# Performance work log

Hardware: AMD Instinct MI355X
Metric: run time of the kernel (lower is better)

Reference implementation:

```python
import jax, jax.numpy as jnp
import numpy as np

B = 131072
D_IN = 128
D_H = 128


def _linear_params(key, fan_in, fan_out):
    # mimic nn.Linear init: U(-1/sqrt(fan_in), 1/sqrt(fan_in))
    kw, kb = jax.random.split(key)
    bound = 1.0 / np.sqrt(fan_in)
    W = jax.random.uniform(kw, (fan_in, fan_out), minval=-bound, maxval=bound, dtype=jnp.float32)
    b = jax.random.uniform(kb, (fan_out,), minval=-bound, maxval=bound, dtype=jnp.float32)
    return W, b


def setup_inputs() -> dict:
    key = jax.random.key(0)
    ks = jax.random.split(key, 12)
    inp = {
        'input': jax.random.normal(ks[0], (B, D_IN), dtype=jnp.float32),
        'seq_input': jax.random.normal(ks[1], (B, D_IN), dtype=jnp.float32),
        'hidden': jax.random.normal(ks[2], (B, D_H), dtype=jnp.float32),
    }
    names = ['ir', 'iz', 'in_', 'sr', 'sz', 'sn', 'hr', 'hz', 'hn']
    for i, nm in enumerate(names):
        fan_in = D_H if nm.startswith('h') else D_IN
        W, b = _linear_params(ks[3 + i], fan_in, D_H)
        inp['W_' + nm] = W
        inp['b_' + nm] = b
    return inp


def reference(input, seq_input, hidden,
              W_ir, b_ir, W_iz, b_iz, W_in_, b_in_,
              W_sr, b_sr, W_sz, b_sz, W_sn, b_sn,
              W_hr, b_hr, W_hz, b_hz, W_hn, b_hn):
    def lin(x, W, b):
        return x @ W + b

    hr = lin(hidden, W_hr, b_hr)  # shared between r_input and r_seq
    r_input = jax.nn.sigmoid(lin(input, W_ir, b_ir) + hr)
    r_seq = jax.nn.sigmoid(lin(seq_input, W_sr, b_sr) + hr)
    r = (r_input + r_seq) * 0.5

    hz = lin(hidden, W_hz, b_hz)
    z_input = jax.nn.sigmoid(lin(input, W_iz, b_iz) + hz)
    z_seq = jax.nn.sigmoid(lin(seq_input, W_sz, b_sz) + hz)
    z = (z_input + z_seq) * 0.5

    n = jnp.tanh(lin(input, W_in_, b_in_) + lin(seq_input, W_sn, b_sn)
                 + lin(r * hidden, W_hn, b_hn))
    new_hidden = (1.0 - z) * n + z * hidden
    return new_hidden
```

## Files before the change

### kernel.cpp

```cpp
#include <hip/hip_runtime.h>

#define BDIM 512
#define PACK_BDIM 256

typedef __attribute__((ext_vector_type(8))) short bf16x8;
typedef __attribute__((ext_vector_type(4))) float f32x4;
typedef __attribute__((ext_vector_type(4))) unsigned int u32x4;

__device__ __forceinline__ unsigned short f2b(float x) {
    unsigned u = __float_as_uint(x);
    return (unsigned short)((u + 0x7fffu + ((u >> 16) & 1u)) >> 16);
}

typedef __attribute__((address_space(1))) const unsigned int ga_u32;
typedef __attribute__((address_space(3))) unsigned int la_u32;
__device__ __forceinline__ void gload_lds16(const void* g, void* l) {
    __builtin_amdgcn_global_load_lds((ga_u32*)g, (la_u32*)l, 16, 0, 0);
}

__global__ __launch_bounds__(PACK_BDIM) void pack_weights(
    const float* __restrict__ w0, const float* __restrict__ w1,
    const float* __restrict__ w2, const float* __restrict__ w3,
    const float* __restrict__ w4, const float* __restrict__ w5,
    const float* __restrict__ w6, const float* __restrict__ w7,
    const float* __restrict__ w8,
    const float* __restrict__ b0, const float* __restrict__ b1,
    const float* __restrict__ b2, const float* __restrict__ b3,
    const float* __restrict__ b4, const float* __restrict__ b5,
    const float* __restrict__ b6, const float* __restrict__ b7,
    const float* __restrict__ b8, unsigned short* __restrict__ wp)
{
    __shared__ float wsm[16384];
    const float* W; const float* Bp;
    switch (blockIdx.x) {
        case 0: W = w0; Bp = b0; break; case 1: W = w1; Bp = b1; break;
        case 2: W = w2; Bp = b2; break; case 3: W = w3; Bp = b3; break;
        case 4: W = w4; Bp = b4; break; case 5: W = w5; Bp = b5; break;
        case 6: W = w6; Bp = b6; break; case 7: W = w7; Bp = b7; break;
        default: W = w8; Bp = b8; break;
    }
    const int tid = threadIdx.x;
    for (int i = tid; i < 16384; i += PACK_BDIM) wsm[i] = W[i];
    float* biasf = (float*)(wp + 147456);
    if (tid < 128) biasf[blockIdx.x * 128 + tid] = Bp[tid];
    __syncthreads();
    unsigned short* dst = wp + (size_t)blockIdx.x * 16384;
    for (int item = tid; item < 2048; item += PACK_BDIM) {
        const int lane = item & 63, cf = item >> 6;
        const int c = cf >> 3, f = cf & 7;
        const int k0 = c * 32 + (lane >> 4) * 8;
        const int n  = f * 16 + (lane & 15);
        u32x4 vv;
        for (int i2 = 0; i2 < 4; i2++) {
            unsigned short lo = f2b(wsm[(k0 + 2 * i2)     * 128 + n]);
            unsigned short hi = f2b(wsm[(k0 + 2 * i2 + 1) * 128 + n]);
            vv[i2] = (unsigned)lo | ((unsigned)hi << 16);
        }
        *(u32x4*)(dst + (size_t)cf * 512 + lane * 8) = vv;
    }
}

__global__ __launch_bounds__(BDIM) __attribute__((amdgpu_waves_per_eu(4)))
void gru_fused(
    const float* __restrict__ inp, const float* __restrict__ seqp,
    const float* __restrict__ hid, const unsigned short* __restrict__ wp,
    float* __restrict__ outp)
{
    __shared__ __align__(16) unsigned short wbuf[2][16384];
    float* tbR = (float*)wbuf[1];
    float* tbO = (float*)wbuf[0];

    const int tid    = threadIdx.x;
    const int lane   = tid & 63;
    const int wid    = tid >> 6;
    const int rowgrp = wid >> 1;
    const int colgrp = wid & 1;
    const int agrp   = lane >> 4;
    const int a16    = lane & 15;
    const int ncol0  = colgrp * 64;
    const size_t row0 = (size_t)blockIdx.x * 64;
    const int locrow_a = rowgrp * 16 + a16;
    const int rswA = (locrow_a & 7) << 3;

    const float* pAin  = inp  + (row0 + locrow_a) * 128;
    const float* pAseq = seqp + (row0 + locrow_a) * 128;
    const float* pAhid = hid  + (row0 + locrow_a) * 128;
    const float* biasf = (const float*)(wp + 147456);

    f32x4 hx[4], s1[4], nacc[4], G[4];
    const f32x4 zv = {0.f, 0.f, 0.f, 0.f};

    auto stageu = [&](int g, int b) {
        const char* src = (const char*)wp + (size_t)g * 32768;
        char* dstb = (char*)wbuf[b];
        #pragma unroll
        for (int j = 0; j < 4; j++) {
            const int off = (j * 8 + wid) * 1024;
            gload_lds16(src + off + lane * 16, dstb + off);
        }
    };

    auto splitc2 = [&](f32x4 x0, f32x4 x1, bf16x8& ah, bf16x8& al) {
        u32x4 a, l;
        #pragma unroll
        for (int p = 0; p < 2; p++) {
            unsigned e0 = __float_as_uint(x0[2 * p]);
            unsigned e1 = __float_as_uint(x0[2 * p + 1]);
            a[p] = __builtin_amdgcn_perm(e1, e0, 0x07060302u);
            float d0 = x0[2 * p]     - __uint_as_float(e0 & 0xffff0000u);
            float d1 = x0[2 * p + 1] - __uint_as_float(e1 & 0xffff0000u);
            l[p] = __builtin_amdgcn_perm(__float_as_uint(d1), __float_as_uint(d0), 0x07060302u);
            unsigned f0 = __float_as_uint(x1[2 * p]);
            unsigned f1 = __float_as_uint(x1[2 * p + 1]);
            a[2 + p] = __builtin_amdgcn_perm(f1, f0, 0x07060302u);
            float g0 = x1[2 * p]     - __uint_as_float(f0 & 0xffff0000u);
            float g1 = x1[2 * p + 1] - __uint_as_float(f1 & 0xffff0000u);
            l[2 + p] = __builtin_amdgcn_perm(__float_as_uint(g1), __float_as_uint(g0), 0x07060302u);
        }
        ah = *(const bf16x8*)&a;
        al = *(const bf16x8*)&l;
    };

    auto gemmG = [&](int b, const float* pA, int g) {
        #pragma unroll
        for (int f = 0; f < 4; f++) G[f] = zv;
        const unsigned short* wb = wbuf[b];
        #pragma unroll
        for (int c = 0; c < 4; c++) {
            const float* p = pA + c * 32 + agrp * 8;
            bf16x8 ah, al;
            splitc2(*(const f32x4*)(p), *(const f32x4*)(p + 4), ah, al);
            __builtin_amdgcn_s_setprio(1);
            #pragma unroll
            for (int f = 0; f < 4; f++) {
                const int fglob = colgrp * 4 + f;
                const bf16x8 w = *(const bf16x8*)(&wb[(size_t)(c * 8 + fglob) * 512 + lane * 8]);
                G[f] = __builtin_amdgcn_mfma_f32_16x16x32_bf16(ah, w, G[f], 0, 0, 0);
                G[f] = __builtin_amdgcn_mfma_f32_16x16x32_bf16(al, w, G[f], 0, 0, 0);
            }
            __builtin_amdgcn_s_setprio(0);
        }
        #pragma unroll
        for (int f = 0; f < 4; f++) {
            float bv = biasf[g * 128 + ncol0 + f * 16 + a16];
            #pragma unroll
            for (int j = 0; j < 4; j++) G[f][j] += bv;
        }
    };

    auto gemmL = [&](int g) {
        #pragma unroll
        for (int f = 0; f < 4; f++) G[f] = zv;
        const unsigned short* wb = wbuf[0];
        #pragma unroll
        for (int c = 0; c < 4; c++) {
            const int rk = (c * 32 + agrp * 8) ^ rswA;
            f32x4 x0 = *(const f32x4*)(&tbR[locrow_a * 128 + rk]);
            f32x4 x1 = *(const f32x4*)(&tbR[locrow_a * 128 + rk + 4]);
            bf16x8 ah, al;
            splitc2(x0, x1, ah, al);
            __builtin_amdgcn_s_setprio(1);
            #pragma unroll
            for (int f = 0; f < 4; f++) {
                const int fglob = colgrp * 4 + f;
                const bf16x8 w = *(const bf16x8*)(&wb[(size_t)(c * 8 + fglob) * 512 + lane * 8]);
                G[f] = __builtin_amdgcn_mfma_f32_16x16x32_bf16(ah, w, G[f], 0, 0, 0);
                G[f] = __builtin_amdgcn_mfma_f32_16x16x32_bf16(al, w, G[f], 0, 0, 0);
            }
            __builtin_amdgcn_s_setprio(0);
        }
        #pragma unroll
        for (int f = 0; f < 4; f++) {
            float bv = biasf[g * 128 + ncol0 + f * 16 + a16];
            #pragma unroll
            for (int j = 0; j < 4; j++) G[f][j] += bv;
        }
    };

    auto sigm = [](float x) { return 1.f / (1.f + __expf(-x)); };
    auto tanh_ = [](float x) {
        x = fminf(18.f, fmaxf(-18.f, x));
        float e = __expf(2.f * x);
        return (e - 1.f) / (e + 1.f);
    };

    const unsigned long long GT = 0x417528306ULL;
    const unsigned CBT = 0x152u;
    stageu(6, 0);

    #pragma clang loop unroll(disable)
    for (int u = 0; u < 9; ++u) {
        const int g = (int)((GT >> (4 * u)) & 15);
        __syncthreads();
        if (u == 3) {
            gemmL(g);
        } else {
            if (u != 2 && u != 8)
                stageu((int)((GT >> (4 * (u + 1))) & 15), (CBT >> (u + 1)) & 1);
            const float* pA = (u == 0 || u == 6) ? pAhid
                            : (u == 1 || u == 4 || u == 7) ? pAin : pAseq;
            gemmG((CBT >> u) & 1, pA, g);
        }
        switch (u) {
            case 0: case 6:
                #pragma unroll
                for (int f = 0; f < 4; f++) hx[f] = G[f];
                break;
            case 1: case 7:
                #pragma unroll
                for (int f = 0; f < 4; f++)
                    #pragma unroll
                    for (int j = 0; j < 4; j++)
                        s1[f][j] = sigm(G[f][j] + hx[f][j]);
                break;
            case 2: {
                #pragma unroll
                for (int f = 0; f < 4; f++)
                    #pragma unroll
                    for (int j = 0; j < 4; j++) {
                        int row = rowgrp * 16 + agrp * 4 + j;
                        int col = ncol0 + f * 16 + a16;
                        float r = 0.5f * (s1[f][j] + sigm(G[f][j] + hx[f][j]));
                        float h = hid[(row0 + row) * 128 + col];
                        tbR[row * 128 + (col ^ ((row & 7) << 3))] = r * h;
                    }
                break;
            }
            case 3:
                #pragma unroll
                for (int f = 0; f < 4; f++) nacc[f] = G[f];
                break;
            case 4: case 5:
                #pragma unroll
                for (int f = 0; f < 4; f++) nacc[f] += G[f];
                break;
            default:
                break;
        }
        if (u == 2) { __syncthreads(); stageu(8, 0); }
        if (u == 3) { __syncthreads(); stageu(2, 1); }
    }

    #pragma unroll
    for (int f = 0; f < 4; f++)
        #pragma unroll
        for (int j = 0; j < 4; j++) {
            int row = rowgrp * 16 + agrp * 4 + j;
            int col = ncol0 + f * 16 + a16;
            float zz = 0.5f * (s1[f][j] + sigm(G[f][j] + hx[f][j]));
            float h  = hid[(row0 + row) * 128 + col];
            float nn = tanh_(nacc[f][j]);
            tbO[row * 128 + (col ^ ((row & 7) << 3))] = (1.f - zz) * nn + zz * h;
        }
    __syncthreads();
    #pragma unroll
    for (int p = 0; p < 4; p++) {
        int e = p * 2048 + tid * 4;
        int rrow = e >> 7, c0 = e & 127;
        f32x4 v = *(const f32x4*)(&tbO[rrow * 128 + (c0 ^ ((rrow & 7) << 3))]);
        *(f32x4*)(&outp[(row0 + rrow) * 128 + c0]) = v;
    }
}

extern "C" void kernel_launch(void* const* d_in, const int* in_sizes, int n_in,
                              void* d_out, int out_size, void* d_ws, size_t ws_size,
                              hipStream_t stream)
{
    (void)in_sizes; (void)n_in; (void)out_size; (void)ws_size;
    const float* inp  = (const float*)d_in[0];
    const float* seqp = (const float*)d_in[1];
    const float* hid  = (const float*)d_in[2];
    const float* W[9]; const float* Bv[9];
    for (int i = 0; i < 9; i++) {
        W[i]  = (const float*)d_in[3 + 2 * i];
        Bv[i] = (const float*)d_in[4 + 2 * i];
    }
    unsigned short* wp = (unsigned short*)d_ws;

    pack_weights<<<9, PACK_BDIM, 0, stream>>>(W[0], W[1], W[2], W[3], W[4],
                                              W[5], W[6], W[7], W[8],
                                              Bv[0], Bv[1], Bv[2], Bv[3], Bv[4],
                                              Bv[5], Bv[6], Bv[7], Bv[8], wp);
    gru_fused<<<2048, BDIM, 0, stream>>>(inp, seqp, hid, wp, (float*)d_out);
}
```

Before: 302.4 us.

## Switch GEMMs from 16x16x32 to 32x32x16 bf16 MFMA tiles

Rewrites the per-wave GEMM tiling to use 32x32x16 MFMA instructions. Each wave now owns a 32-row by 32-column tile instead of 16 rows by 64 columns. The weight pack layout and the epilogue row/column mapping change to match. The aim is fewer A-operand loads and bf16 hi/lo splits per MFMA, and fewer LDS weight reads per wave. In exchange each wave issues a serial chain of 16 dependent MFMAs on a single accumulator, and the s_setprio hints are removed.

```diff
diff --git a/kernel.cpp b/kernel.cpp
--- a/kernel.cpp
+++ b/kernel.cpp
@@ -5,6 +5,7 @@
 
 typedef __attribute__((ext_vector_type(8))) short bf16x8;
 typedef __attribute__((ext_vector_type(4))) float f32x4;
+typedef __attribute__((ext_vector_type(16))) float f32x16;
 typedef __attribute__((ext_vector_type(4))) unsigned int u32x4;
 
 __device__ __forceinline__ unsigned short f2b(float x) {
@@ -46,17 +47,17 @@
     __syncthreads();
     unsigned short* dst = wp + (size_t)blockIdx.x * 16384;
     for (int item = tid; item < 2048; item += PACK_BDIM) {
-        const int lane = item & 63, cf = item >> 6;
-        const int c = cf >> 3, f = cf & 7;
-        const int k0 = c * 32 + (lane >> 4) * 8;
-        const int n  = f * 16 + (lane & 15);
+        const int lane = item & 63, q = item >> 6;
+        const int s = q >> 2, F = q & 3;
+        const int k0 = s * 16 + (lane >> 5) * 8;
+        const int n  = F * 32 + (lane & 31);
         u32x4 vv;
         for (int i2 = 0; i2 < 4; i2++) {
             unsigned short lo = f2b(wsm[(k0 + 2 * i2)     * 128 + n]);
             unsigned short hi = f2b(wsm[(k0 + 2 * i2 + 1) * 128 + n]);
             vv[i2] = (unsigned)lo | ((unsigned)hi << 16);
         }
-        *(u32x4*)(dst + (size_t)cf * 512 + lane * 8) = vv;
+        *(u32x4*)(dst + (size_t)q * 512 + lane * 8) = vv;
     }
 }
 
@@ -73,22 +74,23 @@
     const int tid    = threadIdx.x;
     const int lane   = tid & 63;
     const int wid    = tid >> 6;
-    const int rowgrp = wid >> 1;
-    const int colgrp = wid & 1;
-    const int agrp   = lane >> 4;
-    const int a16    = lane & 15;
-    const int ncol0  = colgrp * 64;
+    const int rowgrp = wid >> 2;
+    const int colgrp = wid & 3;
+    const int l31    = lane & 31;
+    const int kgrp   = lane >> 5;
     const size_t row0 = (size_t)blockIdx.x * 64;
-    const int locrow_a = rowgrp * 16 + a16;
+    const int locrow_a = rowgrp * 32 + l31;
     const int rswA = (locrow_a & 7) << 3;
+    const int ocol = colgrp * 32 + l31;
 
     const float* pAin  = inp  + (row0 + locrow_a) * 128;
     const float* pAseq = seqp + (row0 + locrow_a) * 128;
     const float* pAhid = hid  + (row0 + locrow_a) * 128;
     const float* biasf = (const float*)(wp + 147456);
 
-    f32x4 hx[4], s1[4], nacc[4], G[4];
-    const f32x4 zv = {0.f, 0.f, 0.f, 0.f};
+    f32x16 hx, s1, nacc, G;
+    const f32x16 zv = {0.f,0.f,0.f,0.f,0.f,0.f,0.f,0.f,
+                       0.f,0.f,0.f,0.f,0.f,0.f,0.f,0.f};
 
     auto stageu = [&](int g, int b) {
         const char* src = (const char*)wp + (size_t)g * 32768;
@@ -122,59 +124,39 @@
     };
 
     auto gemmG = [&](int b, const float* pA, int g) {
-        #pragma unroll
-        for (int f = 0; f < 4; f++) G[f] = zv;
+        G = zv;
         const unsigned short* wb = wbuf[b];
         #pragma unroll
-        for (int c = 0; c < 4; c++) {
-            const float* p = pA + c * 32 + agrp * 8;
+        for (int s = 0; s < 8; s++) {
+            const float* p = pA + s * 16 + kgrp * 8;
             bf16x8 ah, al;
-            splitc2(*(const f32x4*)(p), *(const f32x4*)(p + 4), ah, al);
-            __builtin_amdgcn_s_setprio(1);
-            #pragma unroll
-            for (int f = 0; f < 4; f++) {
-                const int fglob = colgrp * 4 + f;
-                const bf16x8 w = *(const bf16x8*)(&wb[(size_t)(c * 8 + fglob) * 512 + lane * 8]);
-                G[f] = __builtin_amdgcn_mfma_f32_16x16x32_bf16(ah, w, G[f], 0, 0, 0);
-                G[f] = __builtin_amdgcn_mfma_f32_16x16x32_bf16(al, w, G[f], 0, 0, 0);
-            }
-            __builtin_amdgcn_s_setprio(0);
-        }
-        #pragma unroll
-        for (int f = 0; f < 4; f++) {
-            float bv = biasf[g * 128 + ncol0 + f * 16 + a16];
-            #pragma unroll
-            for (int j = 0; j < 4; j++) G[f][j] += bv;
-        }
+            splitc2(*(const f32x4*)p, *(const f32x4*)(p + 4), ah, al);
+            const bf16x8 w = *(const bf16x8*)(&wb[(size_t)(s * 4 + colgrp) * 512 + lane * 8]);
+            G = __builtin_amdgcn_mfma_f32_32x32x16_bf16(ah, w, G, 0, 0, 0);
+            G = __builtin_amdgcn_mfma_f32_32x32x16_bf16(al, w, G, 0, 0, 0);
+        }
+        const float bv = biasf[g * 128 + ocol];
+        #pragma unroll
+        for (int r = 0; r < 16; r++) G[r] += bv;
     };
 
     auto gemmL = [&](int g) {
-        #pragma unroll
-        for (int f = 0; f < 4; f++) G[f] = zv;
+        G = zv;
         const unsigned short* wb = wbuf[0];
         #pragma unroll
-        for (int c = 0; c < 4; c++) {
-            const int rk = (c * 32 + agrp * 8) ^ rswA;
+        for (int s = 0; s < 8; s++) {
+            const int rk = (s * 16 + kgrp * 8) ^ rswA;
             f32x4 x0 = *(const f32x4*)(&tbR[locrow_a * 128 + rk]);
             f32x4 x1 = *(const f32x4*)(&tbR[locrow_a * 128 + rk + 4]);
             bf16x8 ah, al;
             splitc2(x0, x1, ah, al);
-            __builtin_amdgcn_s_setprio(1);
-            #pragma unroll
-            for (int f = 0; f < 4; f++) {
-                const int fglob = colgrp * 4 + f;
-                const bf16x8 w = *(const bf16x8*)(&wb[(size_t)(c * 8 + fglob) * 512 + lane * 8]);
-                G[f] = __builtin_amdgcn_mfma_f32_16x16x32_bf16(ah, w, G[f], 0, 0, 0);
-                G[f] = __builtin_amdgcn_mfma_f32_16x16x32_bf16(al, w, G[f], 0, 0, 0);
-            }
-            __builtin_amdgcn_s_setprio(0);
-        }
-        #pragma unroll
-        for (int f = 0; f < 4; f++) {
-            float bv = biasf[g * 128 + ncol0 + f * 16 + a16];
-            #pragma unroll
-            for (int j = 0; j < 4; j++) G[f][j] += bv;
-        }
+            const bf16x8 w = *(const bf16x8*)(&wb[(size_t)(s * 4 + colgrp) * 512 + lane * 8]);
+            G = __builtin_amdgcn_mfma_f32_32x32x16_bf16(ah, w, G, 0, 0, 0);
+            G = __builtin_amdgcn_mfma_f32_32x32x16_bf16(al, w, G, 0, 0, 0);
+        }
+        const float bv = biasf[g * 128 + ocol];
+        #pragma unroll
+        for (int r = 0; r < 16; r++) G[r] += bv;
     };
 
     auto sigm = [](float x) { return 1.f / (1.f + __expf(-x)); };
@@ -203,36 +185,28 @@
         }
         switch (u) {
             case 0: case 6:
-                #pragma unroll
-                for (int f = 0; f < 4; f++) hx[f] = G[f];
+                hx = G;
                 break;
             case 1: case 7:
                 #pragma unroll
-                for (int f = 0; f < 4; f++)
-                    #pragma unroll
-                    for (int j = 0; j < 4; j++)
-                        s1[f][j] = sigm(G[f][j] + hx[f][j]);
+                for (int r = 0; r < 16; r++) s1[r] = sigm(G[r] + hx[r]);
                 break;
             case 2: {
                 #pragma unroll
-                for (int f = 0; f < 4; f++)
-                    #pragma unroll
-                    for (int j = 0; j < 4; j++) {
-                        int row = rowgrp * 16 + agrp * 4 + j;
-                        int col = ncol0 + f * 16 + a16;
-                        float r = 0.5f * (s1[f][j] + sigm(G[f][j] + hx[f][j]));
-                        float h = hid[(row0 + row) * 128 + col];
-                        tbR[row * 128 + (col ^ ((row & 7) << 3))] = r * h;
-                    }
+                for (int r = 0; r < 16; r++) {
+                    int row = rowgrp * 32 + (r & 3) + 8 * (r >> 2) + 4 * kgrp;
+                    float rr = 0.5f * (s1[r] + sigm(G[r] + hx[r]));
+                    float h = hid[(row0 + row) * 128 + ocol];
+                    tbR[row * 128 + (ocol ^ ((row & 7) << 3))] = rr * h;
+                }
                 break;
             }
             case 3:
-                #pragma unroll
-                for (int f = 0; f < 4; f++) nacc[f] = G[f];
+                nacc = G;
                 break;
             case 4: case 5:
                 #pragma unroll
-                for (int f = 0; f < 4; f++) nacc[f] += G[f];
+                for (int r = 0; r < 16; r++) nacc[r] += G[r];
                 break;
             default:
                 break;
@@ -242,16 +216,13 @@
     }
 
     #pragma unroll
-    for (int f = 0; f < 4; f++)
-        #pragma unroll
-        for (int j = 0; j < 4; j++) {
-            int row = rowgrp * 16 + agrp * 4 + j;
-            int col = ncol0 + f * 16 + a16;
-            float zz = 0.5f * (s1[f][j] + sigm(G[f][j] + hx[f][j]));
-            float h  = hid[(row0 + row) * 128 + col];
-            float nn = tanh_(nacc[f][j]);
-            tbO[row * 128 + (col ^ ((row & 7) << 3))] = (1.f - zz) * nn + zz * h;
-        }
+    for (int r = 0; r < 16; r++) {
+        int row = rowgrp * 32 + (r & 3) + 8 * (r >> 2) + 4 * kgrp;
+        float zz = 0.5f * (s1[r] + sigm(G[r] + hx[r]));
+        float h  = hid[(row0 + row) * 128 + ocol];
+        float nn = tanh_(nacc[r]);
+        tbO[row * 128 + (ocol ^ ((row & 7) << 3))] = (1.f - zz) * nn + zz * h;
+    }
     __syncthreads();
     #pragma unroll
     for (int p = 0; p < 4; p++) {
```

Measured after the change: 438.1 us. +44.9%, slower.

## Restructure GRU kernel into 1024-thread blocks with per-wave row tiles and three-slot weight staging

Applied to the files above, without the earlier changes.

Blocks grow to 1024 threads covering 256 rows, and each wave now owns 16 full rows across all 128 columns. Three gate weight matrices are staged into LDS at once, in three phases (r gates, n gates, z gates). The r*h product is kept in registers as a packed hi/lo bf16 pair and moved between lane layouts through per-wave LDS slices, so no block-wide tile exchange is needed. The n value is stored as fp16 until the final combine, and output is written through small per-wave LDS transposes. The aim is to amortise each weight load over more rows and cut block-wide syncs, at the cost of fewer resident blocks and higher register and LDS pressure. Storing n in fp16 also adds a small precision loss.

```diff
diff --git a/kernel.cpp b/kernel.cpp
--- a/kernel.cpp
+++ b/kernel.cpp
@@ -1,11 +1,12 @@
 #include <hip/hip_runtime.h>
 
-#define BDIM 512
+#define BDIM 1024
 #define PACK_BDIM 256
 
 typedef __attribute__((ext_vector_type(8))) short bf16x8;
 typedef __attribute__((ext_vector_type(4))) float f32x4;
 typedef __attribute__((ext_vector_type(4))) unsigned int u32x4;
+typedef __attribute__((ext_vector_type(2))) __fp16 f16x2;
 
 __device__ __forceinline__ unsigned short f2b(float x) {
     unsigned u = __float_as_uint(x);
@@ -66,37 +67,32 @@
     const float* __restrict__ hid, const unsigned short* __restrict__ wp,
     float* __restrict__ outp)
 {
-    __shared__ __align__(16) unsigned short wbuf[2][16384];
-    float* tbR = (float*)wbuf[1];
-    float* tbO = (float*)wbuf[0];
-
-    const int tid    = threadIdx.x;
-    const int lane   = tid & 63;
-    const int wid    = tid >> 6;
-    const int rowgrp = wid >> 1;
-    const int colgrp = wid & 1;
-    const int agrp   = lane >> 4;
-    const int a16    = lane & 15;
-    const int ncol0  = colgrp * 64;
-    const size_t row0 = (size_t)blockIdx.x * 64;
-    const int locrow_a = rowgrp * 16 + a16;
-    const int rswA = (locrow_a & 7) << 3;
-
-    const float* pAin  = inp  + (row0 + locrow_a) * 128;
-    const float* pAseq = seqp + (row0 + locrow_a) * 128;
-    const float* pAhid = hid  + (row0 + locrow_a) * 128;
+    __shared__ __align__(16) unsigned short wbuf[3][16384];
+    __shared__ __align__(16) float tscr[8192];
+
+    const int tid  = threadIdx.x;
+    const int lane = tid & 63;
+    const int wid  = tid >> 6;
+    const int a16  = lane & 15;
+    const int agrp = lane >> 4;
+    const size_t row0 = (size_t)blockIdx.x * 256 + wid * 16;
+
+    const float* pAin  = inp  + (row0 + a16) * 128;
+    const float* pAseq = seqp + (row0 + a16) * 128;
+    const float* pAhid = hid  + (row0 + a16) * 128;
     const float* biasf = (const float*)(wp + 147456);
 
-    f32x4 hx[4], s1[4], nacc[4], G[4];
-    const f32x4 zv = {0.f, 0.f, 0.f, 0.f};
-
-    auto stageu = [&](int g, int b) {
-        const char* src = (const char*)wp + (size_t)g * 32768;
-        char* dstb = (char*)wbuf[b];
-        #pragma unroll
-        for (int j = 0; j < 4; j++) {
-            const int off = (j * 8 + wid) * 1024;
-            gload_lds16(src + off + lane * 16, dstb + off);
+    auto stage3 = [&](int ga, int gb, int gc) {
+        const int gs[3] = {ga, gb, gc};
+        #pragma unroll
+        for (int s = 0; s < 3; s++) {
+            const char* src = (const char*)wp + (size_t)gs[s] * 32768;
+            char* dst = (char*)wbuf[s];
+            #pragma unroll
+            for (int j = 0; j < 2; j++) {
+                const int off = (j * 16 + wid) * 1024;
+                gload_lds16(src + off + lane * 16, dst + off);
+            }
         }
     };
 
@@ -121,59 +117,41 @@
         al = *(const bf16x8*)&l;
     };
 
-    auto gemmG = [&](int b, const float* pA, int g) {
-        #pragma unroll
-        for (int f = 0; f < 4; f++) G[f] = zv;
-        const unsigned short* wb = wbuf[b];
+    auto gemmHalf = [&](int slot, const float* pA, int hb4, f32x4* acc) {
+        #pragma unroll
+        for (int f = 0; f < 4; f++) acc[f] = (f32x4){0.f, 0.f, 0.f, 0.f};
+        const unsigned short* wb = wbuf[slot];
         #pragma unroll
         for (int c = 0; c < 4; c++) {
             const float* p = pA + c * 32 + agrp * 8;
             bf16x8 ah, al;
-            splitc2(*(const f32x4*)(p), *(const f32x4*)(p + 4), ah, al);
+            splitc2(*(const f32x4*)p, *(const f32x4*)(p + 4), ah, al);
             __builtin_amdgcn_s_setprio(1);
             #pragma unroll
-            for (int f = 0; f < 4; f++) {
-                const int fglob = colgrp * 4 + f;
-                const bf16x8 w = *(const bf16x8*)(&wb[(size_t)(c * 8 + fglob) * 512 + lane * 8]);
-                G[f] = __builtin_amdgcn_mfma_f32_16x16x32_bf16(ah, w, G[f], 0, 0, 0);
-                G[f] = __builtin_amdgcn_mfma_f32_16x16x32_bf16(al, w, G[f], 0, 0, 0);
+            for (int fl = 0; fl < 4; fl++) {
+                const bf16x8 w = *(const bf16x8*)(&wb[(size_t)(c * 8 + hb4 + fl) * 512 + lane * 8]);
+                acc[fl] = __builtin_amdgcn_mfma_f32_16x16x32_bf16(ah, w, acc[fl], 0, 0, 0);
+                acc[fl] = __builtin_amdgcn_mfma_f32_16x16x32_bf16(al, w, acc[fl], 0, 0, 0);
             }
             __builtin_amdgcn_s_setprio(0);
         }
-        #pragma unroll
-        for (int f = 0; f < 4; f++) {
-            float bv = biasf[g * 128 + ncol0 + f * 16 + a16];
-            #pragma unroll
-            for (int j = 0; j < 4; j++) G[f][j] += bv;
-        }
-    };
-
-    auto gemmL = [&](int g) {
-        #pragma unroll
-        for (int f = 0; f < 4; f++) G[f] = zv;
-        const unsigned short* wb = wbuf[0];
+    };
+
+    auto gemmFull = [&](int slot, const float* pA, f32x4* acc8) {
+        const unsigned short* wb = wbuf[slot];
         #pragma unroll
         for (int c = 0; c < 4; c++) {
-            const int rk = (c * 32 + agrp * 8) ^ rswA;
-            f32x4 x0 = *(const f32x4*)(&tbR[locrow_a * 128 + rk]);
-            f32x4 x1 = *(const f32x4*)(&tbR[locrow_a * 128 + rk + 4]);
+            const float* p = pA + c * 32 + agrp * 8;
             bf16x8 ah, al;
-            splitc2(x0, x1, ah, al);
+            splitc2(*(const f32x4*)p, *(const f32x4*)(p + 4), ah, al);
             __builtin_amdgcn_s_setprio(1);
             #pragma unroll
-            for (int f = 0; f < 4; f++) {
-                const int fglob = colgrp * 4 + f;
-                const bf16x8 w = *(const bf16x8*)(&wb[(size_t)(c * 8 + fglob) * 512 + lane * 8]);
-                G[f] = __builtin_amdgcn_mfma_f32_16x16x32_bf16(ah, w, G[f], 0, 0, 0);
-                G[f] = __builtin_amdgcn_mfma_f32_16x16x32_bf16(al, w, G[f], 0, 0, 0);
+            for (int f = 0; f < 8; f++) {
+                const bf16x8 w = *(const bf16x8*)(&wb[(size_t)(c * 8 + f) * 512 + lane * 8]);
+                acc8[f] = __builtin_amdgcn_mfma_f32_16x16x32_bf16(ah, w, acc8[f], 0, 0, 0);
+                acc8[f] = __builtin_amdgcn_mfma_f32_16x16x32_bf16(al, w, acc8[f], 0, 0, 0);
             }
             __builtin_amdgcn_s_setprio(0);
-        }
-        #pragma unroll
-        for (int f = 0; f < 4; f++) {
-            float bv = biasf[g * 128 + ncol0 + f * 16 + a16];
-            #pragma unroll
-            for (int j = 0; j < 4; j++) G[f][j] += bv;
         }
     };
 
@@ -184,81 +162,168 @@
         return (e - 1.f) / (e + 1.f);
     };
 
-    const unsigned long long GT = 0x417528306ULL;
-    const unsigned CBT = 0x152u;
-    stageu(6, 0);
-
-    #pragma clang loop unroll(disable)
-    for (int u = 0; u < 9; ++u) {
-        const int g = (int)((GT >> (4 * u)) & 15);
-        __syncthreads();
-        if (u == 3) {
-            gemmL(g);
-        } else {
-            if (u != 2 && u != 8)
-                stageu((int)((GT >> (4 * (u + 1))) & 15), (CBT >> (u + 1)) & 1);
-            const float* pA = (u == 0 || u == 6) ? pAhid
-                            : (u == 1 || u == 4 || u == 7) ? pAin : pAseq;
-            gemmG((CBT >> u) & 1, pA, g);
-        }
-        switch (u) {
-            case 0: case 6:
+    stage3(6, 0, 3);
+    __syncthreads();
+    unsigned rhp[32];
+    #pragma unroll
+    for (int half = 0; half < 2; half++) {
+        f32x4 hx[4], s1[4], G[4];
+        gemmHalf(0, pAhid, half * 4, hx);
+        gemmHalf(1, pAin,  half * 4, G);
+        #pragma unroll
+        for (int fl = 0; fl < 4; fl++) {
+            const int col = half * 64 + fl * 16 + a16;
+            const float bh = biasf[6 * 128 + col];
+            const float bi = biasf[0 * 128 + col];
+            #pragma unroll
+            for (int j = 0; j < 4; j++) {
+                hx[fl][j] += bh;
+                s1[fl][j] = sigm(G[fl][j] + bi + hx[fl][j]);
+            }
+        }
+        gemmHalf(2, pAseq, half * 4, G);
+        #pragma unroll
+        for (int fl = 0; fl < 4; fl++) {
+            const int col = half * 64 + fl * 16 + a16;
+            const float bs = biasf[3 * 128 + col];
+            #pragma unroll
+            for (int j = 0; j < 4; j++) {
+                const int rowC = agrp * 4 + j;
+                float rr = 0.5f * (s1[fl][j] + sigm(G[fl][j] + bs + hx[fl][j]));
+                float h  = hid[(row0 + rowC) * 128 + col];
+                float rh = rr * h;
+                unsigned u = __float_as_uint(rh);
+                float rem = rh - __uint_as_float(u & 0xffff0000u);
+                rhp[half * 16 + fl * 4 + j] = (u & 0xffff0000u) | (__float_as_uint(rem) >> 16);
+            }
+        }
+    }
+
+    __syncthreads();
+    unsigned* slice = (wid < 12) ? ((unsigned*)wbuf) + wid * 2048
+                                 : ((unsigned*)tscr) + (wid - 12) * 2048;
+    #pragma unroll
+    for (int half = 0; half < 2; half++)
+        #pragma unroll
+        for (int fl = 0; fl < 4; fl++)
+            #pragma unroll
+            for (int j = 0; j < 4; j++) {
+                const int rowC = agrp * 4 + j;
+                const int col  = half * 64 + fl * 16 + a16;
+                const int swb  = ((rowC & 7) << 3) | ((rowC & 8) >> 1);
+                slice[rowC * 128 + (col ^ swb)] = rhp[half * 16 + fl * 4 + j];
+            }
+    u32x4 rha[8];
+    {
+        const int swb = ((a16 & 7) << 3) | ((a16 & 8) >> 1);
+        #pragma unroll
+        for (int c = 0; c < 4; c++) {
+            const int k0 = c * 32 + agrp * 8;
+            rha[c * 2]     = *(const u32x4*)&slice[a16 * 128 + (k0 ^ swb)];
+            rha[c * 2 + 1] = *(const u32x4*)&slice[a16 * 128 + ((k0 + 4) ^ swb)];
+        }
+    }
+    __syncthreads();
+
+    stage3(8, 2, 5);
+    __syncthreads();
+    f32x4 nacc[8];
+    #pragma unroll
+    for (int f = 0; f < 8; f++) nacc[f] = (f32x4){0.f, 0.f, 0.f, 0.f};
+    {
+        const unsigned short* wb = wbuf[0];
+        #pragma unroll
+        for (int c = 0; c < 4; c++) {
+            const u32x4 lo = rha[c * 2], hi = rha[c * 2 + 1];
+            u32x4 av, lv;
+            av[0] = __builtin_amdgcn_perm(lo[1], lo[0], 0x07060302u);
+            av[1] = __builtin_amdgcn_perm(lo[3], lo[2], 0x07060302u);
+            av[2] = __builtin_amdgcn_perm(hi[1], hi[0], 0x07060302u);
+            av[3] = __builtin_amdgcn_perm(hi[3], hi[2], 0x07060302u);
+            lv[0] = __builtin_amdgcn_perm(lo[1], lo[0], 0x05040100u);
+            lv[1] = __builtin_amdgcn_perm(lo[3], lo[2], 0x05040100u);
+            lv[2] = __builtin_amdgcn_perm(hi[1], hi[0], 0x05040100u);
+            lv[3] = __builtin_amdgcn_perm(hi[3], hi[2], 0x05040100u);
+            const bf16x8 ah = *(const bf16x8*)&av;
+            const bf16x8 al = *(const bf16x8*)&lv;
+            __builtin_amdgcn_s_setprio(1);
+            #pragma unroll
+            for (int f = 0; f < 8; f++) {
+                const bf16x8 w = *(const bf16x8*)(&wb[(size_t)(c * 8 + f) * 512 + lane * 8]);
+                nacc[f] = __builtin_amdgcn_mfma_f32_16x16x32_bf16(ah, w, nacc[f], 0, 0, 0);
+                nacc[f] = __builtin_amdgcn_mfma_f32_16x16x32_bf16(al, w, nacc[f], 0, 0, 0);
+            }
+            __builtin_amdgcn_s_setprio(0);
+        }
+    }
+    gemmFull(1, pAin,  nacc);
+    gemmFull(2, pAseq, nacc);
+    unsigned nh[16];
+    #pragma unroll
+    for (int f = 0; f < 8; f++) {
+        const int col = f * 16 + a16;
+        const float bs = biasf[8 * 128 + col] + biasf[2 * 128 + col] + biasf[5 * 128 + col];
+        #pragma unroll
+        for (int p = 0; p < 2; p++) {
+            float t0 = tanh_(nacc[f][2 * p]     + bs);
+            float t1 = tanh_(nacc[f][2 * p + 1] + bs);
+            f16x2 pk = __builtin_amdgcn_cvt_pkrtz(t0, t1);
+            nh[f * 2 + p] = *(unsigned*)&pk;
+        }
+    }
+    __syncthreads();
+
+    stage3(7, 1, 4);
+    __syncthreads();
+    #pragma unroll
+    for (int half = 0; half < 2; half++) {
+        f32x4 hx[4], s1[4], G[4];
+        gemmHalf(0, pAhid, half * 4, hx);
+        gemmHalf(1, pAin,  half * 4, G);
+        #pragma unroll
+        for (int fl = 0; fl < 4; fl++) {
+            const int col = half * 64 + fl * 16 + a16;
+            const float bh = biasf[7 * 128 + col];
+            const float bi = biasf[1 * 128 + col];
+            #pragma unroll
+            for (int j = 0; j < 4; j++) {
+                hx[fl][j] += bh;
+                s1[fl][j] = sigm(G[fl][j] + bi + hx[fl][j]);
+            }
+        }
+        gemmHalf(2, pAseq, half * 4, G);
+        float* oslice = &tscr[wid * 512];
+        #pragma unroll
+        for (int q = 0; q < 2; q++) {
+            #pragma unroll
+            for (int flq = 0; flq < 2; flq++) {
+                const int fl = q * 2 + flq;
+                const int col = half * 64 + fl * 16 + a16;
+                const float bz = biasf[4 * 128 + col];
                 #pragma unroll
-                for (int f = 0; f < 4; f++) hx[f] = G[f];
-                break;
-            case 1: case 7:
-                #pragma unroll
-                for (int f = 0; f < 4; f++)
-                    #pragma unroll
-                    for (int j = 0; j < 4; j++)
-                        s1[f][j] = sigm(G[f][j] + hx[f][j]);
-                break;
-            case 2: {
-                #pragma unroll
-                for (int f = 0; f < 4; f++)
-                    #pragma unroll
-                    for (int j = 0; j < 4; j++) {
-                        int row = rowgrp * 16 + agrp * 4 + j;
-                        int col = ncol0 + f * 16 + a16;
-                        float r = 0.5f * (s1[f][j] + sigm(G[f][j] + hx[f][j]));
-                        float h = hid[(row0 + row) * 128 + col];
-                        tbR[row * 128 + (col ^ ((row & 7) << 3))] = r * h;
-                    }
-                break;
-            }
-            case 3:
-                #pragma unroll
-                for (int f = 0; f < 4; f++) nacc[f] = G[f];
-                break;
-            case 4: case 5:
-                #pragma unroll
-                for (int f = 0; f < 4; f++) nacc[f] += G[f];
-                break;
-            default:
-                break;
-        }
-        if (u == 2) { __syncthreads(); stageu(8, 0); }
-        if (u == 3) { __syncthreads(); stageu(2, 1); }
-    }
-
-    #pragma unroll
-    for (int f = 0; f < 4; f++)
-        #pragma unroll
-        for (int j = 0; j < 4; j++) {
-            int row = rowgrp * 16 + agrp * 4 + j;
-            int col = ncol0 + f * 16 + a16;
-            float zz = 0.5f * (s1[f][j] + sigm(G[f][j] + hx[f][j]));
-            float h  = hid[(row0 + row) * 128 + col];
-            float nn = tanh_(nacc[f][j]);
-            tbO[row * 128 + (col ^ ((row & 7) << 3))] = (1.f - zz) * nn + zz * h;
-        }
-    __syncthreads();
-    #pragma unroll
-    for (int p = 0; p < 4; p++) {
-        int e = p * 2048 + tid * 4;
-        int rrow = e >> 7, c0 = e & 127;
-        f32x4 v = *(const f32x4*)(&tbO[rrow * 128 + (c0 ^ ((rrow & 7) << 3))]);
-        *(f32x4*)(&outp[(row0 + rrow) * 128 + c0]) = v;
+                for (int j = 0; j < 4; j++) {
+                    const int rowC = agrp * 4 + j;
+                    float z = 0.5f * (s1[fl][j] + sigm(G[fl][j] + bz + hx[fl][j]));
+                    float h = hid[(row0 + rowC) * 128 + col];
+                    unsigned nv = nh[(half * 4 + fl) * 2 + (j >> 1)];
+                    unsigned short us = (j & 1) ? (unsigned short)(nv >> 16)
+                                                : (unsigned short)(nv & 0xffffu);
+                    __fp16 hf; __builtin_memcpy(&hf, &us, 2);
+                    float n = (float)hf;
+                    float o = n + z * (h - n);
+                    const int cq = flq * 16 + a16;
+                    oslice[rowC * 32 + (cq ^ ((rowC & 7) << 2))] = o;
+                }
+            }
+            const int r16 = lane >> 2;
+            const int c8  = (lane & 3) * 8;
+            const int sw  = (r16 & 7) << 2;
+            f32x4 v0 = *(const f32x4*)&oslice[r16 * 32 + (c8 ^ sw)];
+            f32x4 v1 = *(const f32x4*)&oslice[r16 * 32 + ((c8 + 4) ^ sw)];
+            float* po = outp + (row0 + r16) * 128 + half * 64 + q * 32 + c8;
+            *(f32x4*)po = v0;
+            *(f32x4*)(po + 4) = v1;
+        }
     }
 }
 
@@ -281,5 +346,5 @@
                                               W[5], W[6], W[7], W[8],
                                               Bv[0], Bv[1], Bv[2], Bv[3], Bv[4],
                                               Bv[5], Bv[6], Bv[7], Bv[8], wp);
-    gru_fused<<<2048, BDIM, 0, stream>>>(inp, seqp, hid, wp, (float*)d_out);
-}
+    gru_fused<<<512, BDIM, 0, stream>>>(inp, seqp, hid, wp, (float*)d_out);
+}
```

Result: slower. 434.8 us (+43.8%).
